# Kernel optimization log

Hardware: AMD Instinct MI355X
Metric: run time of the kernel (lower is better)

Reference implementation:

```python
import jax, jax.numpy as jnp
from jax import lax
import numpy as np

B, T, D, H, K = 16, 2048, 512, 512, 2

def setup_inputs() -> dict:
    key = jax.random.key(0)
    k1, k2, k3 = jax.random.split(key, 3)
    inputs = jax.random.normal(k1, (B, T, D), dtype=jnp.float32)
    conv_w = jax.random.normal(k2, (3 * H, D, K), dtype=jnp.float32) * (1.0 / np.sqrt(D * K))
    conv_b = jax.random.normal(k3, (3 * H,), dtype=jnp.float32) * 0.01
    return {"inputs": inputs, "conv_w": conv_w, "conv_b": conv_b}

def reference(inputs, conv_w, conv_b):
    # inputs: [B, T, D]; conv_w: [3H, D, K]; causal conv via left-pad K-1
    k = conv_w.shape[-1]
    h = conv_w.shape[0] // 3
    x = jnp.transpose(inputs, (0, 2, 1))                      # [B, D, T]
    x = jnp.pad(x, ((0, 0), (0, 0), (k - 1, 0)))              # left pad
    gates = lax.conv_general_dilated(
        x, conv_w, window_strides=(1,), padding='VALID',
        dimension_numbers=('NCH', 'OIH', 'NCH'))              # [B, 3H, T]
    gates = jnp.transpose(gates, (0, 2, 1)) + conv_b          # [B, T, 3H]
    Z, F, O = jnp.split(gates, 3, axis=2)
    Z = jnp.tanh(Z)
    F = jax.nn.sigmoid(F)
    O = jax.nn.sigmoid(O)

    # fo-pool: c_t = f_t * c_{t-1} + (1 - f_t) * z_t, c_{-1} = 0
    def step(c, zf):
        z, f = zf
        c_ = f * c + (1.0 - f) * z
        return c_, c_

    c0 = jnp.zeros((Z.shape[0], h), dtype=Z.dtype)
    _, C = lax.scan(step, c0, (jnp.swapaxes(Z, 0, 1), jnp.swapaxes(F, 0, 1)))
    C = jnp.swapaxes(C, 0, 1)                                 # [B, T, H]
    return C, O * C
```

## Files before the change

kernel.cpp:

```cpp
#include <hip/hip_runtime.h>


#define MTOT 32768
#define NTOT 1536
#define KTOT 1024
#define DCH  512
#define TLEN 2048
#define NB   16

#define HT 32
#define SC 8
#define LC 256

typedef __bf16 bf16x8 __attribute__((ext_vector_type(8)));
typedef float  f32x4  __attribute__((ext_vector_type(4)));

__device__ __forceinline__ unsigned short f2bf(float x) {
    unsigned u = __float_as_uint(x);
    u += 0x7FFFu + ((u >> 16) & 1u);
    return (unsigned short)(u >> 16);
}
__device__ __forceinline__ float bf2f(unsigned short h) {
    return __uint_as_float(((unsigned)h) << 16);
}
__device__ __forceinline__ float sigmoidf_(float x) {
    return 1.f / (1.f + __expf(-x));
}

__global__ __launch_bounds__(256) void make_A(const float* __restrict__ in,
                                              unsigned short* __restrict__ A) {
    size_t i = (size_t)blockIdx.x * 256 + threadIdx.x;
    size_t e = i * 8;
    size_t m = e >> 10;
    int    j = (int)(e & 1023);
    alignas(16) unsigned short h[8];
    if (((m & (TLEN - 1)) == 0) && (j < DCH)) {
#pragma unroll
        for (int r = 0; r < 8; ++r) h[r] = 0;
    } else {
        const float* src = in + ((long long)m - 1) * DCH + j;
        float4 a = *(const float4*)src;
        float4 b = *(const float4*)(src + 4);
        h[0] = f2bf(a.x); h[1] = f2bf(a.y); h[2] = f2bf(a.z); h[3] = f2bf(a.w);
        h[4] = f2bf(b.x); h[5] = f2bf(b.y); h[6] = f2bf(b.z); h[7] = f2bf(b.w);
    }
    *(int4*)(A + e) = *(const int4*)h;
}

__global__ __launch_bounds__(256) void make_B(const float* __restrict__ w,
                                              unsigned short* __restrict__ Bt) {
    int i = blockIdx.x * 256 + threadIdx.x;
    int o = i >> 9, d = i & 511;
    float w0 = w[(size_t)(o * 512 + d) * 2];
    float w1 = w[(size_t)(o * 512 + d) * 2 + 1];
    Bt[(size_t)o * 1024 + d]       = f2bf(w0);
    Bt[(size_t)o * 1024 + 512 + d] = f2bf(w1);
}

__global__ __launch_bounds__(256) void gemm_gates(const unsigned short* __restrict__ A,
                                                  const unsigned short* __restrict__ B,
                                                  const float* __restrict__ bias,
                                                  unsigned short* __restrict__ GT) {
    __shared__ int4 sA[512];
    __shared__ int4 sB[512];

    const int tid = threadIdx.x;
    const int bx  = blockIdx.x;
    const int mT  = bx / 12, nT = bx % 12;
    const int m0  = mT * 128, n0 = nT * 128;

    const int mloc = tid >> 2;
    const int qsw  = (tid & 3) ^ ((mloc >> 1) & 3);
    const unsigned short* ga0 = A + (size_t)(m0 + mloc) * 1024 + qsw * 8;
    const unsigned short* ga1 = A + (size_t)(m0 + 64 + mloc) * 1024 + qsw * 8;
    const unsigned short* gb0 = B + (size_t)(n0 + mloc) * 1024 + qsw * 8;
    const unsigned short* gb1 = B + (size_t)(n0 + 64 + mloc) * 1024 + qsw * 8;

    char* la0 = (char*)sA + tid * 16;
    char* la1 = (char*)sA + 4096 + tid * 16;
    char* lb0 = (char*)sB + tid * 16;
    char* lb1 = (char*)sB + 4096 + tid * 16;

    const int lane = tid & 63;
    const int wv   = tid >> 6;
    const int wm   = (wv & 1) * 64, wn = (wv >> 1) * 64;
    const int lr   = lane & 15, lq = lane >> 4;

    int sAidx[4], sBidx[4];
#pragma unroll
    for (int i = 0; i < 4; ++i) {
        int mi = wm + 16 * i + lr;
        sAidx[i] = mi * 4 + (lq ^ ((mi >> 1) & 3));
        int ni = wn + 16 * i + lr;
        sBidx[i] = ni * 4 + (lq ^ ((ni >> 1) & 3));
    }

    f32x4 acc[4][4] = {};

    for (int kt = 0; kt < KTOT; kt += 32) {
        __builtin_amdgcn_global_load_lds(
            (__attribute__((address_space(1))) void*)(void*)ga0,
            (__attribute__((address_space(3))) void*)la0, 16, 0, 0);
        __builtin_amdgcn_global_load_lds(
            (__attribute__((address_space(1))) void*)(void*)ga1,
            (__attribute__((address_space(3))) void*)la1, 16, 0, 0);
        __builtin_amdgcn_global_load_lds(
            (__attribute__((address_space(1))) void*)(void*)gb0,
            (__attribute__((address_space(3))) void*)lb0, 16, 0, 0);
        __builtin_amdgcn_global_load_lds(
            (__attribute__((address_space(1))) void*)(void*)gb1,
            (__attribute__((address_space(3))) void*)lb1, 16, 0, 0);
        ga0 += 32; ga1 += 32; gb0 += 32; gb1 += 32;
        __syncthreads();

        bf16x8 af[4], bfr[4];
#pragma unroll
        for (int i = 0; i < 4; ++i) af[i]  = __builtin_bit_cast(bf16x8, sA[sAidx[i]]);
#pragma unroll
        for (int j = 0; j < 4; ++j) bfr[j] = __builtin_bit_cast(bf16x8, sB[sBidx[j]]);

#pragma unroll
        for (int i = 0; i < 4; ++i)
#pragma unroll
            for (int j = 0; j < 4; ++j)
                acc[i][j] = __builtin_amdgcn_mfma_f32_16x16x32_bf16(af[i], bfr[j],
                                                                    acc[i][j], 0, 0, 0);
        __syncthreads();
    }

#pragma unroll
    for (int j = 0; j < 4; ++j) {
        int gn = n0 + wn + 16 * j + lr;
        float bj = bias[gn];
#pragma unroll
        for (int i = 0; i < 4; ++i) {
            int rowb = m0 + wm + 16 * i + lq * 4;
            alignas(8) unsigned short pk[4];
#pragma unroll
            for (int r = 0; r < 4; ++r) pk[r] = f2bf(acc[i][j][r] + bj);
            *(int2*)(GT + (size_t)gn * MTOT + rowb) = *(const int2*)pk;
        }
    }
}

__global__ __launch_bounds__(256) void scan_fo(const unsigned short* __restrict__ GT,
                                               float* __restrict__ out) {
    __shared__ float lP[SC][HT];
    __shared__ float lC[SC][HT];
    __shared__ float lI[SC][HT];

    const int tid   = threadIdx.x;
    const int h_loc = tid & (HT - 1);
    const int s     = tid >> 5;
    const int b     = blockIdx.x >> 4;
    const int h0    = (blockIdx.x & 15) * HT;
    const int h     = h0 + h_loc;

    const size_t mbase = (size_t)b * TLEN + (size_t)s * LC;
    const unsigned short* gz = GT + (size_t)h * MTOT + mbase;
    const unsigned short* gf = GT + (size_t)(DCH + h) * MTOT + mbase;
    const unsigned short* go = GT + (size_t)(2 * DCH + h) * MTOT + mbase;

    float P = 1.f, c = 0.f;
    for (int k = 0; k < LC; k += 8) {
        bf16x8 zv = *(const bf16x8*)(gz + k);
        bf16x8 fv = *(const bf16x8*)(gf + k);
#pragma unroll
        for (int r = 0; r < 8; ++r) {
            float f = sigmoidf_((float)fv[r]);
            float z = 2.f * sigmoidf_(2.f * (float)zv[r]) - 1.f;
            c = f * c + (1.f - f) * z;
            P *= f;
        }
    }
    lP[s][h_loc] = P;
    lC[s][h_loc] = c;
    __syncthreads();

    if (tid < HT) {
        float cc = 0.f;
#pragma unroll
        for (int ss = 0; ss < SC; ++ss) {
            lI[ss][tid] = cc;
            cc = lP[ss][tid] * cc + lC[ss][tid];
        }
    }
    __syncthreads();

    c = lI[s][h_loc];
    const size_t BTH = (size_t)NB * TLEN * DCH;
    float* oC  = out + mbase * DCH + h;
    float* oOC = oC + BTH;
    for (int k = 0; k < LC; k += 8) {
        bf16x8 zv = *(const bf16x8*)(gz + k);
        bf16x8 fv = *(const bf16x8*)(gf + k);
        bf16x8 ov = *(const bf16x8*)(go + k);
#pragma unroll
        for (int r = 0; r < 8; ++r) {
            float f = sigmoidf_((float)fv[r]);
            float z = 2.f * sigmoidf_(2.f * (float)zv[r]) - 1.f;
            float o = sigmoidf_((float)ov[r]);
            c = f * c + (1.f - f) * z;
            oC[(size_t)(k + r) * DCH]  = c;
            oOC[(size_t)(k + r) * DCH] = o * c;
        }
    }
}

extern "C" void kernel_launch(void* const* d_in, const int* in_sizes, int n_in,
                              void* d_out, int out_size, void* d_ws, size_t ws_size,
                              hipStream_t stream) {
    const float* in   = (const float*)d_in[0];
    const float* w    = (const float*)d_in[1];
    const float* bias = (const float*)d_in[2];
    float* out = (float*)d_out;

    unsigned short* Abf = (unsigned short*)d_ws;
    unsigned short* Bbf = Abf + (size_t)MTOT * 1024;
    unsigned short* GT  = Bbf + (size_t)NTOT * 1024;

    make_A<<<dim3(16384), dim3(256), 0, stream>>>(in, Abf);
    make_B<<<dim3(3072),  dim3(256), 0, stream>>>(w, Bbf);
    gemm_gates<<<dim3(3072), dim3(256), 0, stream>>>(Abf, Bbf, bias, GT);
    scan_fo<<<dim3(NB * (DCH / HT)), dim3(256), 0, stream>>>(GT, out);
}
```

Before: 407.3 us.

## Split fo-pool scan into three kernels with finer chunks and XCD-aware GEMM tiling

The single scan kernel becomes three: a per-chunk aggregate pass, a cross-chunk carry scan and an apply pass. Chunks shrink from 256 to 64 timesteps, so many more threads walk the sequential recurrence in parallel. GEMM block indices are remapped so each XCD gets a contiguous band of M tiles, which should improve L2 reuse. The cost is two extra launches and a global-memory round trip for the chunk carries. P, C and I are placed at the start of the workspace, which overlaps the bf16 A buffer; this is safe only because A is dead once the GEMM finishes.

```diff
diff --git a/kernel.cpp b/kernel.cpp
--- a/kernel.cpp
+++ b/kernel.cpp
@@ -8,9 +8,8 @@
 #define TLEN 2048
 #define NB   16
 
-#define HT 32
-#define SC 8
-#define LC 256
+#define SC 32
+#define LC 64
 
 typedef __bf16 bf16x8 __attribute__((ext_vector_type(8)));
 typedef float  f32x4  __attribute__((ext_vector_type(4)));
@@ -19,9 +18,6 @@
     unsigned u = __float_as_uint(x);
     u += 0x7FFFu + ((u >> 16) & 1u);
     return (unsigned short)(u >> 16);
-}
-__device__ __forceinline__ float bf2f(unsigned short h) {
-    return __uint_as_float(((unsigned)h) << 16);
 }
 __device__ __forceinline__ float sigmoidf_(float x) {
     return 1.f / (1.f + __expf(-x));
@@ -66,7 +62,10 @@
 
     const int tid = threadIdx.x;
     const int bx  = blockIdx.x;
-    const int mT  = bx / 12, nT = bx % 12;
+    const int xcd = bx & 7;
+    const int i2  = bx >> 3;
+    const int mT  = xcd * 32 + i2 / 12;
+    const int nT  = i2 % 12;
     const int m0  = mT * 128, n0 = nT * 128;
 
     const int mloc = tid >> 2;
@@ -143,25 +142,16 @@
     }
 }
 
-__global__ __launch_bounds__(256) void scan_fo(const unsigned short* __restrict__ GT,
-                                               float* __restrict__ out) {
-    __shared__ float lP[SC][HT];
-    __shared__ float lC[SC][HT];
-    __shared__ float lI[SC][HT];
-
-    const int tid   = threadIdx.x;
-    const int h_loc = tid & (HT - 1);
-    const int s     = tid >> 5;
-    const int b     = blockIdx.x >> 4;
-    const int h0    = (blockIdx.x & 15) * HT;
-    const int h     = h0 + h_loc;
-
-    const size_t mbase = (size_t)b * TLEN + (size_t)s * LC;
-    const unsigned short* gz = GT + (size_t)h * MTOT + mbase;
-    const unsigned short* gf = GT + (size_t)(DCH + h) * MTOT + mbase;
-    const unsigned short* go = GT + (size_t)(2 * DCH + h) * MTOT + mbase;
-
-    float P = 1.f, c = 0.f;
+__global__ __launch_bounds__(256) void scan_agg(const unsigned short* __restrict__ GT,
+                                                float* __restrict__ P,
+                                                float* __restrict__ C) {
+    int idx = blockIdx.x * 256 + threadIdx.x;
+    int h = idx & 511, s = (idx >> 9) & 31, b = idx >> 14;
+    const unsigned short* gz = GT + (size_t)h * MTOT + (size_t)b * TLEN + s * LC;
+    const unsigned short* gf = gz + (size_t)DCH * MTOT;
+
+    float p = 1.f, c = 0.f;
+#pragma unroll 2
     for (int k = 0; k < LC; k += 8) {
         bf16x8 zv = *(const bf16x8*)(gz + k);
         bf16x8 fv = *(const bf16x8*)(gf + k);
@@ -170,27 +160,43 @@
             float f = sigmoidf_((float)fv[r]);
             float z = 2.f * sigmoidf_(2.f * (float)zv[r]) - 1.f;
             c = f * c + (1.f - f) * z;
-            P *= f;
+            p *= f;
         }
     }
-    lP[s][h_loc] = P;
-    lC[s][h_loc] = c;
-    __syncthreads();
-
-    if (tid < HT) {
-        float cc = 0.f;
-#pragma unroll
-        for (int ss = 0; ss < SC; ++ss) {
-            lI[ss][tid] = cc;
-            cc = lP[ss][tid] * cc + lC[ss][tid];
-        }
-    }
-    __syncthreads();
-
-    c = lI[s][h_loc];
+    P[idx] = p;
+    C[idx] = c;
+}
+
+__global__ __launch_bounds__(256) void scan_chunks(const float* __restrict__ P,
+                                                   const float* __restrict__ C,
+                                                   float* __restrict__ I) {
+    int j = blockIdx.x * 256 + threadIdx.x;
+    int b = j >> 9, h = j & 511;
+    size_t base = (size_t)b * (SC * DCH) + h;
+    float cc = 0.f;
+#pragma unroll
+    for (int s = 0; s < SC; ++s) {
+        size_t o = base + (size_t)s * DCH;
+        I[o] = cc;
+        cc = P[o] * cc + C[o];
+    }
+}
+
+__global__ __launch_bounds__(256) void scan_apply(const unsigned short* __restrict__ GT,
+                                                  const float* __restrict__ I,
+                                                  float* __restrict__ out) {
+    int idx = blockIdx.x * 256 + threadIdx.x;
+    int h = idx & 511, s = (idx >> 9) & 31, b = idx >> 14;
+    const unsigned short* gz = GT + (size_t)h * MTOT + (size_t)b * TLEN + s * LC;
+    const unsigned short* gf = gz + (size_t)DCH * MTOT;
+    const unsigned short* go = gf + (size_t)DCH * MTOT;
+
     const size_t BTH = (size_t)NB * TLEN * DCH;
-    float* oC  = out + mbase * DCH + h;
+    float* oC  = out + ((size_t)b * TLEN + s * LC) * DCH + h;
     float* oOC = oC + BTH;
+
+    float c = I[idx];
+#pragma unroll 2
     for (int k = 0; k < LC; k += 8) {
         bf16x8 zv = *(const bf16x8*)(gz + k);
         bf16x8 fv = *(const bf16x8*)(gf + k);
@@ -219,8 +225,14 @@
     unsigned short* Bbf = Abf + (size_t)MTOT * 1024;
     unsigned short* GT  = Bbf + (size_t)NTOT * 1024;
 
+    float* P = (float*)d_ws;
+    float* C = P + (size_t)NB * SC * DCH;
+    float* I = C + (size_t)NB * SC * DCH;
+
     make_A<<<dim3(16384), dim3(256), 0, stream>>>(in, Abf);
     make_B<<<dim3(3072),  dim3(256), 0, stream>>>(w, Bbf);
     gemm_gates<<<dim3(3072), dim3(256), 0, stream>>>(Abf, Bbf, bias, GT);
-    scan_fo<<<dim3(NB * (DCH / HT)), dim3(256), 0, stream>>>(GT, out);
-}
+    scan_agg<<<dim3(1024), dim3(256), 0, stream>>>(GT, P, C);
+    scan_chunks<<<dim3(32), dim3(256), 0, stream>>>(P, C, I);
+    scan_apply<<<dim3(1024), dim3(256), 0, stream>>>(GT, I, out);
+}
```

Result: slower. 427.1 us (+4.8%).
